# Kernel optimization log

Measured on AMD Instinct MI355X. Metric: run time of the kernel, lower is better.

Reference implementation:

```python
import jax, jax.numpy as jnp
import numpy as np
from jax import lax

EPS = 1e-5  # torch BatchNorm1d default eps

def _conv(x, w, stride):
    # x: [B,H,W,Cin], w: [3,3,Cin,Cout], padding=1
    return lax.conv_general_dilated(x, w, (stride, stride), ((1, 1), (1, 1)),
                                    dimension_numbers=('NHWC', 'HWIO', 'NHWC'))

def _masked_bn(f, m, gamma, beta):
    # BatchNorm1d over active voxels only (training-mode, biased var),
    # matching BN applied to spconv's [N_active, C] feature matrix.
    # f: [B,H,W,C], m: [B,H,W,1] in {0,1}
    cnt = jnp.sum(m)
    mean = jnp.sum(f * m, axis=(0, 1, 2)) / cnt            # [C]
    var = jnp.sum(m * (f - mean) ** 2, axis=(0, 1, 2)) / cnt
    return ((f - mean) * lax.rsqrt(var + EPS) * gamma + beta) * m

def setup_inputs() -> dict:
    key = jax.random.key(0)
    ks = jax.random.split(key, 4)
    B, H, W, Cin, Cout = 4, 256, 256, 64, 128
    x = jax.random.normal(ks[0], (B, H, W, Cin), dtype=jnp.float32)
    mask = jax.random.randint(ks[1], (B, H, W), 0, 10, dtype=jnp.int32)
    w1 = jax.random.normal(ks[2], (3, 3, Cin, Cout), dtype=jnp.float32) * 0.05
    w2 = jax.random.normal(ks[3], (3, 3, Cout, Cout), dtype=jnp.float32) * 0.05
    gamma1 = jnp.ones((Cout,), jnp.float32)
    beta1 = jnp.zeros((Cout,), jnp.float32)
    gamma2 = jnp.ones((Cout,), jnp.float32)
    beta2 = jnp.zeros((Cout,), jnp.float32)
    return {"x": x, "mask": mask, "w1": w1, "gamma1": gamma1, "beta1": beta1,
            "w2": w2, "gamma2": gamma2, "beta2": beta2}

def reference(x, mask, w1, gamma1, beta1, w2, gamma2, beta2):
    act = (mask == 0).astype(x.dtype)[..., None]   # [B,H,W,1] input active sites
    xm = x * act                                   # sparse tensor densified (zeros off-sites)
    # conv1: regular sparse conv, stride 2 -> output active where any input in 3x3 recep. field
    out = _conv(xm, w1, 2)
    m1 = (_conv(act, jnp.ones((3, 3, 1, 1), x.dtype), 2) > 0).astype(x.dtype)
    out = _masked_bn(out, m1, gamma1, beta1)
    out = jax.nn.relu(out)
    # conv2: submanifold conv, stride 1 -> active set preserved (m1)
    out = _conv(out, w2, 1) * m1
    out = _masked_bn(out, m1, gamma2, beta2)
    return out
```

## Files before the change

### kernel.cpp

```cpp
#include <hip/hip_runtime.h>

#define EPS_BN 1e-5f
#define MFMA16 __builtin_amdgcn_mfma_f32_16x16x32_bf16

typedef unsigned char uchar;
typedef short short8 __attribute__((ext_vector_type(8)));
typedef float f32x4 __attribute__((ext_vector_type(4)));

__device__ __forceinline__ ushort f2bf(float f) {
    unsigned u = __float_as_uint(f);
    return (ushort)((u + 0x7FFFu + ((u >> 16) & 1u)) >> 16);
}
__device__ __forceinline__ float bf2f(ushort h) {
    return __uint_as_float(((unsigned)h) << 16);
}
__device__ __forceinline__ void gload_lds16(const void* g, void* l) {
    __builtin_amdgcn_global_load_lds(
        (const __attribute__((address_space(1))) void*)g,
        (__attribute__((address_space(3))) void*)l, 16, 0, 0);
}


__global__ __launch_bounds__(256) void mask_kernel(const int* __restrict__ mask,
                                                   uchar* __restrict__ m1,
                                                   int* __restrict__ cnt)
{
    int idx = blockIdx.x * 256 + threadIdx.x;
    int ow = idx & 127;
    int oh = (idx >> 7) & 127;
    int b  = idx >> 14;
    bool act = false;
    #pragma unroll
    for (int kh = 0; kh < 3; ++kh) {
        int ih = 2*oh - 1 + kh;
        if ((unsigned)ih >= 256u) continue;
        #pragma unroll
        for (int kw = 0; kw < 3; ++kw) {
            int iw = 2*ow - 1 + kw;
            if ((unsigned)iw >= 256u) continue;
            if (mask[(b*256 + ih)*256 + iw] == 0) act = true;
        }
    }
    m1[idx] = act ? 1 : 0;
    unsigned long long bal = __ballot(act);
    if ((threadIdx.x & 63) == 0)
        atomicAdd(cnt, (int)__popcll(bal));
}

__global__ __launch_bounds__(256) void wcvt_kernel(const float* __restrict__ w1,
                                                   const float* __restrict__ w2,
                                                   ushort* __restrict__ w1T,
                                                   ushort* __restrict__ w2T)
{
    int idx = blockIdx.x * 256 + threadIdx.x;
    if (idx < 73728) {
        int ci = idx & 63;
        int co = (idx >> 6) & 127;
        int s  = idx >> 13;
        w1T[idx] = f2bf(w1[(s*64 + ci)*128 + co]);
    } else if (idx < 221184) {
        int i  = idx - 73728;
        int ci = i & 127;
        int co = (i >> 7) & 127;
        int s  = i >> 14;
        w2T[i] = f2bf(w2[(s*128 + ci)*128 + co]);
    }
}

__global__ __launch_bounds__(512) void conv1_mfma(const float* __restrict__ x,
                                                  const int* __restrict__ mask,
                                                  const ushort* __restrict__ w1T,
                                                  const uchar* __restrict__ m1,
                                                  ushort* __restrict__ out1,
                                                  float* __restrict__ stats)
{
    __shared__ ushort Ah[2 * 258 * 64];
    __shared__ ushort Bd[2][8192];

    const int t     = threadIdx.x;
    const int lane  = t & 63;
    const int wv    = t >> 6;
    const int wbase = t & ~63;
    const int bid   = blockIdx.x;
    const int L     = (bid & 7) * 32 + (bid >> 3);
    const int g     = L & 63;
    const int b     = L >> 6;

    const int wm = wv >> 1, wn = wv & 1;
    const int lr = lane & 15, lg = lane >> 4;

    auto stageA = [&](int kh) {
        for (int idx = t; idx < 4128; idx += 512) {
            int r   = idx >= 2064;
            int rem = idx - r*2064;
            int c = rem >> 3, k = rem & 7;
            int iw = c - 1;
            int ih = 4*g + 2*r + kh - 1;
            short8 v = {0,0,0,0,0,0,0,0};
            if ((unsigned)ih < 256u && (unsigned)iw < 256u) {
                const int* mr = mask + (size_t)(b*256 + ih) * 256;
                if (mr[iw] == 0) {
                    const float* p = x + ((size_t)(b*256 + ih)*256 + iw)*64 + k*8;
                    float4 fa = *(const float4*)p;
                    float4 fb = *(const float4*)(p + 4);
                    v[0]=(short)f2bf(fa.x); v[1]=(short)f2bf(fa.y);
                    v[2]=(short)f2bf(fa.z); v[3]=(short)f2bf(fa.w);
                    v[4]=(short)f2bf(fb.x); v[5]=(short)f2bf(fb.y);
                    v[6]=(short)f2bf(fb.z); v[7]=(short)f2bf(fb.w);
                }
            }
            int ad = ((r*258 + c)*128 + k*16) ^ ((((unsigned)c >> 1) & 7) << 4);
            *(short8*)((char*)Ah + ad) = v;
        }
    };
    const int coB = t >> 3;
    const int kB  = t & 7;
    auto dmaB = [&](int buf, int tap) {
        #pragma unroll
        for (int r = 0; r < 2; ++r) {
            int co = r*64 + coB;
            const ushort* gp = w1T + (size_t)tap*8192 + (size_t)co*64
                             + ((kB ^ (co & 7)) << 3);
            gload_lds16(gp, &Bd[buf][(size_t)(r*512 + wbase)*8]);
        }
    };

    f32x4 acc[4][4];
    #pragma unroll
    for (int mi = 0; mi < 4; ++mi)
        #pragma unroll
        for (int ni = 0; ni < 4; ++ni)
            acc[mi][ni] = (f32x4){0.f, 0.f, 0.f, 0.f};

    stageA(0);
    dmaB(0, 0);
    __syncthreads();

    for (int kt = 0; kt < 9; ++kt) {
        const int kw = kt % 3, cb = kt & 1;
        if (kt < 8) dmaB(cb ^ 1, kt + 1);
        const char* Ab = (const char*)Ah;
        const char* Bb = (const char*)Bd[cb];
        __builtin_amdgcn_s_setprio(1);
        #pragma unroll
        for (int ks = 0; ks < 2; ++ks) {
            short8 af[4], bfr[4];
            #pragma unroll
            for (int mi = 0; mi < 4; ++mi) {
                int px = wm*64 + mi*16 + lr;
                int r  = px >> 7, ow = px & 127;
                int c  = 2*ow + kw;
                af[mi] = *(const short8*)(Ab +
                    (((r*258 + c)*128 + ks*64 + lg*16) ^ ((((unsigned)c >> 1) & 7) << 4)));
            }
            #pragma unroll
            for (int ni = 0; ni < 4; ++ni) {
                int co = wn*64 + ni*16 + lr;
                bfr[ni] = *(const short8*)(Bb +
                    ((co*128 + ks*64 + lg*16) ^ ((co & 7) << 4)));
            }
            #pragma unroll
            for (int mi = 0; mi < 4; ++mi)
                #pragma unroll
                for (int ni = 0; ni < 4; ++ni)
                    acc[mi][ni] = MFMA16(af[mi], bfr[ni], acc[mi][ni], 0, 0, 0);
        }
        __builtin_amdgcn_s_setprio(0);
        __syncthreads();
        if (kw == 2 && kt < 8) {
            stageA(kt/3 + 1);
            __syncthreads();
        }
    }

    const size_t pixbase = (size_t)(b*128 + 2*g) * 128;
    #pragma unroll
    for (int mi = 0; mi < 4; ++mi) {
        #pragma unroll
        for (int ni = 0; ni < 4; ++ni) {
            int p  = wm*64 + mi*16 + lg*4;
            int co = wn*64 + ni*16 + lr;
            #pragma unroll
            for (int r = 0; r < 4; ++r)
                out1[(pixbase + p + r)*128 + co] = f2bf(acc[mi][ni][r]);
        }
    }

    float s4[4] = {0.f,0.f,0.f,0.f}, q4[4] = {0.f,0.f,0.f,0.f};
    #pragma unroll
    for (int mi = 0; mi < 4; ++mi) {
        const uchar* mp = m1 + pixbase + wm*64 + mi*16 + lg*4;
        #pragma unroll
        for (int r = 0; r < 4; ++r) {
            float a = mp[r] ? 1.f : 0.f;
            #pragma unroll
            for (int ni = 0; ni < 4; ++ni) {
                float av = a * acc[mi][ni][r];
                s4[ni] += av;
                q4[ni] += av * acc[mi][ni][r];
            }
        }
    }
    float* red = (float*)Ah;
    const int rrow = wm*4 + lg;
    #pragma unroll
    for (int ni = 0; ni < 4; ++ni) {
        red[rrow*128 + wn*64 + ni*16 + lr]        = s4[ni];
        red[2048 + rrow*128 + wn*64 + ni*16 + lr] = q4[ni];
    }
    __syncthreads();
    if (t < 128) {
        float v = 0.f, q = 0.f;
        #pragma unroll
        for (int rr = 0; rr < 16; ++rr) { v += red[rr*128 + t]; q += red[2048 + rr*128 + t]; }
        atomicAdd(&stats[t], v);
        atomicAdd(&stats[128 + t], q);
    }
}

__global__ __launch_bounds__(512) void conv2_mfma(const ushort* __restrict__ a,
                                                  const ushort* __restrict__ w2T,
                                                  const uchar* __restrict__ m1,
                                                  const float* __restrict__ sb,
                                                  float* __restrict__ outraw,
                                                  float* __restrict__ stats)
{
    __shared__ ushort Ah[2 * 130 * 128];
    __shared__ ushort Bd[2][8192];
    __shared__ float scb[256];

    const int t     = threadIdx.x;
    const int lane  = t & 63;
    const int wv    = t >> 6;
    const int wbase = t & ~63;
    const int bid   = blockIdx.x;
    const int L     = (bid & 7) * 32 + (bid >> 3);
    const int g     = L & 63;
    const int b     = L >> 6;

    const int wm = wv >> 1, wn = wv & 1;
    const int lr = lane & 15, lg = lane >> 4;

    if (t < 256) scb[t] = sb[t];

    auto stageA = [&](int kh) {
        for (int idx = t; idx < 4160; idx += 512) {
            int r   = idx >= 2080;
            int rem = idx - r*2080;
            int c = rem >> 4, k = rem & 15;
            int iw = c - 1;
            int ih = 2*g + r + kh - 1;
            short8 v = {0,0,0,0,0,0,0,0};
            if ((unsigned)ih < 128u && (unsigned)iw < 128u) {
                const uchar* mr = m1 + (size_t)(b*128 + ih) * 128;
                if (mr[iw]) {
                    short8 rv = *(const short8*)(a + ((size_t)(b*128 + ih)*128 + iw)*128 + k*8);
                    #pragma unroll
                    for (int j = 0; j < 8; ++j) {
                        float f = fmaf(bf2f((ushort)rv[j]), scb[k*8 + j], scb[128 + k*8 + j]);
                        v[j] = (short)f2bf(fmaxf(f, 0.f));
                    }
                }
            }
            int ad = ((r*130 + c)*256 + k*16) ^ ((c & 7) << 4);
            *(short8*)((char*)Ah + ad) = v;
        }
    };
    const int coB = t >> 3;
    const int kB  = t & 7;
    auto dmaB = [&](int buf, int kt) {
        const int s = kt / 6, j = kt % 6;
        const int tap = s*3 + (j >> 1);
        const int h = j & 1;
        #pragma unroll
        for (int r = 0; r < 2; ++r) {
            int co = r*64 + coB;
            const ushort* gp = w2T + (size_t)tap*16384 + (size_t)co*128 + h*64
                             + ((kB ^ (co & 7)) << 3);
            gload_lds16(gp, &Bd[buf][(size_t)(r*512 + wbase)*8]);
        }
    };

    f32x4 acc[4][4];
    #pragma unroll
    for (int mi = 0; mi < 4; ++mi)
        #pragma unroll
        for (int ni = 0; ni < 4; ++ni)
            acc[mi][ni] = (f32x4){0.f, 0.f, 0.f, 0.f};

    __syncthreads();
    stageA(0);
    dmaB(0, 0);
    __syncthreads();

    for (int kt = 0; kt < 18; ++kt) {
        const int j = kt % 6;
        const int kw = j >> 1, h = j & 1, cb = kt & 1;
        if (kt < 17) dmaB(cb ^ 1, kt + 1);
        const char* Ab = (const char*)Ah;
        const char* Bb = (const char*)Bd[cb];
        __builtin_amdgcn_s_setprio(1);
        #pragma unroll
        for (int ks = 0; ks < 2; ++ks) {
            short8 af[4], bfr[4];
            #pragma unroll
            for (int mi = 0; mi < 4; ++mi) {
                int px = wm*64 + mi*16 + lr;
                int r  = px >> 7, ow = px & 127;
                int c  = ow + kw;
                af[mi] = *(const short8*)(Ab +
                    (((r*130 + c)*256 + h*128 + ks*64 + lg*16) ^ ((c & 7) << 4)));
            }
            #pragma unroll
            for (int ni = 0; ni < 4; ++ni) {
                int co = wn*64 + ni*16 + lr;
                bfr[ni] = *(const short8*)(Bb +
                    ((co*128 + ks*64 + lg*16) ^ ((co & 7) << 4)));
            }
            #pragma unroll
            for (int mi = 0; mi < 4; ++mi)
                #pragma unroll
                for (int ni = 0; ni < 4; ++ni)
                    acc[mi][ni] = MFMA16(af[mi], bfr[ni], acc[mi][ni], 0, 0, 0);
        }
        __builtin_amdgcn_s_setprio(0);
        __syncthreads();
        if (j == 5 && kt < 17) {
            stageA(kt/6 + 1);
            __syncthreads();
        }
    }

    const size_t pixbase = (size_t)(b*128 + 2*g) * 128;
    #pragma unroll
    for (int mi = 0; mi < 4; ++mi) {
        #pragma unroll
        for (int ni = 0; ni < 4; ++ni) {
            int p  = wm*64 + mi*16 + lg*4;
            int co = wn*64 + ni*16 + lr;
            #pragma unroll
            for (int r = 0; r < 4; ++r)
                outraw[(pixbase + p + r)*128 + co] = acc[mi][ni][r];
        }
    }

    float s4[4] = {0.f,0.f,0.f,0.f}, q4[4] = {0.f,0.f,0.f,0.f};
    #pragma unroll
    for (int mi = 0; mi < 4; ++mi) {
        const uchar* mp = m1 + pixbase + wm*64 + mi*16 + lg*4;
        #pragma unroll
        for (int r = 0; r < 4; ++r) {
            float a0 = mp[r] ? 1.f : 0.f;
            #pragma unroll
            for (int ni = 0; ni < 4; ++ni) {
                float av = a0 * acc[mi][ni][r];
                s4[ni] += av;
                q4[ni] += av * acc[mi][ni][r];
            }
        }
    }
    float* red = (float*)Ah;
    const int rrow = wm*4 + lg;
    #pragma unroll
    for (int ni = 0; ni < 4; ++ni) {
        red[rrow*128 + wn*64 + ni*16 + lr]        = s4[ni];
        red[2048 + rrow*128 + wn*64 + ni*16 + lr] = q4[ni];
    }
    __syncthreads();
    if (t < 128) {
        float v = 0.f, q = 0.f;
        #pragma unroll
        for (int rr = 0; rr < 16; ++rr) { v += red[rr*128 + t]; q += red[2048 + rr*128 + t]; }
        atomicAdd(&stats[t], v);
        atomicAdd(&stats[128 + t], q);
    }
}

__global__ void finalize_kernel(const float* __restrict__ stats,
                                const float* __restrict__ gamma,
                                const float* __restrict__ beta,
                                float* __restrict__ sbout,
                                const int* __restrict__ cnt)
{
    int c = threadIdx.x;
    float n = (float)(*cnt);
    float mean = stats[c] / n;
    float var  = stats[128 + c] / n - mean*mean;
    var = fmaxf(var, 0.f);
    float scale = gamma[c] * rsqrtf(var + EPS_BN);
    sbout[c]       = scale;
    sbout[128 + c] = beta[c] - mean*scale;
}

__global__ __launch_bounds__(256) void apply_kernel(float* __restrict__ out,
                                                    const uchar* __restrict__ m1,
                                                    const float* __restrict__ sb)
{
    int idx4 = blockIdx.x * 256 + threadIdx.x;
    int pos = idx4 >> 5;
    int c4  = (idx4 & 31) << 2;
    float4 v = ((const float4*)out)[idx4];
    float4 r = make_float4(0.f, 0.f, 0.f, 0.f);
    if (m1[pos]) {
        r.x = fmaf(v.x, sb[c4+0], sb[128+c4+0]);
        r.y = fmaf(v.y, sb[c4+1], sb[128+c4+1]);
        r.z = fmaf(v.z, sb[c4+2], sb[128+c4+2]);
        r.w = fmaf(v.w, sb[c4+3], sb[128+c4+3]);
    }
    ((float4*)out)[idx4] = r;
}

extern "C" void kernel_launch(void* const* d_in, const int* in_sizes, int n_in,
                              void* d_out, int out_size, void* d_ws, size_t ws_size,
                              hipStream_t stream)
{
    const float* x      = (const float*)d_in[0];
    const int*   mask   = (const int*)d_in[1];
    const float* w1     = (const float*)d_in[2];
    const float* gamma1 = (const float*)d_in[3];
    const float* beta1  = (const float*)d_in[4];
    const float* w2     = (const float*)d_in[5];
    const float* gamma2 = (const float*)d_in[6];
    const float* beta2  = (const float*)d_in[7];

    ushort* out1 = (ushort*)d_ws;
    ushort* w1T  = out1 + 8388608;
    ushort* w2T  = w1T + 73728;
    float* stats = (float*)(w2T + 147456);
    float* sb    = stats + 512;
    int*   cnt   = (int*)(sb + 512);
    uchar* m1    = (uchar*)(cnt + 4);

    float* out = (float*)d_out;

    hipMemsetAsync(stats, 0, 1024*sizeof(float) + 4*sizeof(int), stream);

    mask_kernel <<<256, 256, 0, stream>>>(mask, m1, cnt);
    wcvt_kernel <<<864, 256, 0, stream>>>(w1, w2, w1T, w2T);
    conv1_mfma  <<<256, 512, 0, stream>>>(x, mask, w1T, m1, out1, stats);
    finalize_kernel<<<1, 128, 0, stream>>>(stats, gamma1, beta1, sb, cnt);
    conv2_mfma  <<<256, 512, 0, stream>>>(out1, w2T, m1, sb, out, stats + 256);
    finalize_kernel<<<1, 128, 0, stream>>>(stats + 256, gamma2, beta2, sb + 256, cnt);
    apply_kernel<<<8192, 256, 0, stream>>>(out, m1, sb + 256);
}
```

Baseline: 112.0 us.

## Split conv blocks to one output row each with 256 threads and 512 blocks

Both conv kernels now handle a single output row per block (128 pixels) with 4 waves instead of two rows with 8 waves. The grid doubles to 512 blocks, LDS for the A tile is halved, and the weight DMA is spread over 4 issues per thread. The main loops are fully unrolled and bf16 conversion now uses the HIP library intrinsic. This aims to fill more CUs (256 CUs on MI355X) and raise occupancy, at the cost of loading each weight tile twice as often per output pixel.

```diff
diff --git a/kernel.cpp b/kernel.cpp
--- a/kernel.cpp
+++ b/kernel.cpp
@@ -1,4 +1,5 @@
 #include <hip/hip_runtime.h>
+#include <hip/hip_bf16.h>
 
 #define EPS_BN 1e-5f
 #define MFMA16 __builtin_amdgcn_mfma_f32_16x16x32_bf16
@@ -8,8 +9,8 @@
 typedef float f32x4 __attribute__((ext_vector_type(4)));
 
 __device__ __forceinline__ ushort f2bf(float f) {
-    unsigned u = __float_as_uint(f);
-    return (ushort)((u + 0x7FFFu + ((u >> 16) & 1u)) >> 16);
+    __hip_bfloat16 h = __float2bfloat16(f);
+    return *(ushort*)&h;
 }
 __device__ __forceinline__ float bf2f(ushort h) {
     return __uint_as_float(((unsigned)h) << 16);
@@ -67,14 +68,14 @@
     }
 }
 
-__global__ __launch_bounds__(512) void conv1_mfma(const float* __restrict__ x,
+__global__ __launch_bounds__(256) void conv1_mfma(const float* __restrict__ x,
                                                   const int* __restrict__ mask,
                                                   const ushort* __restrict__ w1T,
                                                   const uchar* __restrict__ m1,
                                                   ushort* __restrict__ out1,
                                                   float* __restrict__ stats)
 {
-    __shared__ ushort Ah[2 * 258 * 64];
+    __shared__ ushort Ah[258 * 64];
     __shared__ ushort Bd[2][8192];
 
     const int t     = threadIdx.x;
@@ -82,34 +83,33 @@
     const int wv    = t >> 6;
     const int wbase = t & ~63;
     const int bid   = blockIdx.x;
-    const int L     = (bid & 7) * 32 + (bid >> 3);
-    const int g     = L & 63;
-    const int b     = L >> 6;
+    const int L     = (bid & 7) * 64 + (bid >> 3);
+    const int oh    = L & 127;
+    const int b     = L >> 7;
 
     const int wm = wv >> 1, wn = wv & 1;
     const int lr = lane & 15, lg = lane >> 4;
 
     auto stageA = [&](int kh) {
-        for (int idx = t; idx < 4128; idx += 512) {
-            int r   = idx >= 2064;
-            int rem = idx - r*2064;
-            int c = rem >> 3, k = rem & 7;
+        int ih = 2*oh + kh - 1;
+        bool rok = ((unsigned)ih < 256u);
+        int ihc = ih < 0 ? 0 : (ih > 255 ? 255 : ih);
+        const float* xr = x + (size_t)(b*256 + ihc) * 256 * 64;
+        const int*   mr = mask + (size_t)(b*256 + ihc) * 256;
+        for (int idx = t; idx < 2064; idx += 256) {
+            int c = idx >> 3, k = idx & 7;
             int iw = c - 1;
-            int ih = 4*g + 2*r + kh - 1;
             short8 v = {0,0,0,0,0,0,0,0};
-            if ((unsigned)ih < 256u && (unsigned)iw < 256u) {
-                const int* mr = mask + (size_t)(b*256 + ih) * 256;
-                if (mr[iw] == 0) {
-                    const float* p = x + ((size_t)(b*256 + ih)*256 + iw)*64 + k*8;
-                    float4 fa = *(const float4*)p;
-                    float4 fb = *(const float4*)(p + 4);
-                    v[0]=(short)f2bf(fa.x); v[1]=(short)f2bf(fa.y);
-                    v[2]=(short)f2bf(fa.z); v[3]=(short)f2bf(fa.w);
-                    v[4]=(short)f2bf(fb.x); v[5]=(short)f2bf(fb.y);
-                    v[6]=(short)f2bf(fb.z); v[7]=(short)f2bf(fb.w);
-                }
-            }
-            int ad = ((r*258 + c)*128 + k*16) ^ ((((unsigned)c >> 1) & 7) << 4);
+            if (rok && (unsigned)iw < 256u && mr[iw] == 0) {
+                const float* p = xr + (size_t)iw*64 + k*8;
+                float4 fa = *(const float4*)p;
+                float4 fb = *(const float4*)(p + 4);
+                v[0]=(short)f2bf(fa.x); v[1]=(short)f2bf(fa.y);
+                v[2]=(short)f2bf(fa.z); v[3]=(short)f2bf(fa.w);
+                v[4]=(short)f2bf(fb.x); v[5]=(short)f2bf(fb.y);
+                v[6]=(short)f2bf(fb.z); v[7]=(short)f2bf(fb.w);
+            }
+            int ad = (c*128 + k*16) ^ ((((unsigned)c >> 1) & 7) << 4);
             *(short8*)((char*)Ah + ad) = v;
         }
     };
@@ -117,11 +117,11 @@
     const int kB  = t & 7;
     auto dmaB = [&](int buf, int tap) {
         #pragma unroll
-        for (int r = 0; r < 2; ++r) {
-            int co = r*64 + coB;
+        for (int r = 0; r < 4; ++r) {
+            int co = r*32 + coB;
             const ushort* gp = w1T + (size_t)tap*8192 + (size_t)co*64
                              + ((kB ^ (co & 7)) << 3);
-            gload_lds16(gp, &Bd[buf][(size_t)(r*512 + wbase)*8]);
+            gload_lds16(gp, &Bd[buf][(size_t)(r*256 + wbase)*8]);
         }
     };
 
@@ -136,6 +136,7 @@
     dmaB(0, 0);
     __syncthreads();
 
+    #pragma unroll
     for (int kt = 0; kt < 9; ++kt) {
         const int kw = kt % 3, cb = kt & 1;
         if (kt < 8) dmaB(cb ^ 1, kt + 1);
@@ -148,10 +149,9 @@
             #pragma unroll
             for (int mi = 0; mi < 4; ++mi) {
                 int px = wm*64 + mi*16 + lr;
-                int r  = px >> 7, ow = px & 127;
-                int c  = 2*ow + kw;
+                int c  = 2*px + kw;
                 af[mi] = *(const short8*)(Ab +
-                    (((r*258 + c)*128 + ks*64 + lg*16) ^ ((((unsigned)c >> 1) & 7) << 4)));
+                    ((c*128 + ks*64 + lg*16) ^ ((((unsigned)c >> 1) & 7) << 4)));
             }
             #pragma unroll
             for (int ni = 0; ni < 4; ++ni) {
@@ -173,7 +173,7 @@
         }
     }
 
-    const size_t pixbase = (size_t)(b*128 + 2*g) * 128;
+    const size_t pixbase = (size_t)(b*128 + oh) * 128;
     #pragma unroll
     for (int mi = 0; mi < 4; ++mi) {
         #pragma unroll
@@ -206,26 +206,26 @@
     #pragma unroll
     for (int ni = 0; ni < 4; ++ni) {
         red[rrow*128 + wn*64 + ni*16 + lr]        = s4[ni];
-        red[2048 + rrow*128 + wn*64 + ni*16 + lr] = q4[ni];
+        red[1024 + rrow*128 + wn*64 + ni*16 + lr] = q4[ni];
     }
     __syncthreads();
     if (t < 128) {
         float v = 0.f, q = 0.f;
         #pragma unroll
-        for (int rr = 0; rr < 16; ++rr) { v += red[rr*128 + t]; q += red[2048 + rr*128 + t]; }
+        for (int rr = 0; rr < 8; ++rr) { v += red[rr*128 + t]; q += red[1024 + rr*128 + t]; }
         atomicAdd(&stats[t], v);
         atomicAdd(&stats[128 + t], q);
     }
 }
 
-__global__ __launch_bounds__(512) void conv2_mfma(const ushort* __restrict__ a,
+__global__ __launch_bounds__(256) void conv2_mfma(const ushort* __restrict__ a,
                                                   const ushort* __restrict__ w2T,
                                                   const uchar* __restrict__ m1,
                                                   const float* __restrict__ sb,
                                                   float* __restrict__ outraw,
                                                   float* __restrict__ stats)
 {
-    __shared__ ushort Ah[2 * 130 * 128];
+    __shared__ ushort Ah[130 * 128];
     __shared__ ushort Bd[2][8192];
     __shared__ float scb[256];
 
@@ -234,35 +234,34 @@
     const int wv    = t >> 6;
     const int wbase = t & ~63;
     const int bid   = blockIdx.x;
-    const int L     = (bid & 7) * 32 + (bid >> 3);
-    const int g     = L & 63;
-    const int b     = L >> 6;
+    const int L     = (bid & 7) * 64 + (bid >> 3);
+    const int oh    = L & 127;
+    const int b     = L >> 7;
 
     const int wm = wv >> 1, wn = wv & 1;
     const int lr = lane & 15, lg = lane >> 4;
 
-    if (t < 256) scb[t] = sb[t];
+    scb[t & 255] = sb[t & 255];
 
     auto stageA = [&](int kh) {
-        for (int idx = t; idx < 4160; idx += 512) {
-            int r   = idx >= 2080;
-            int rem = idx - r*2080;
-            int c = rem >> 4, k = rem & 15;
+        int ih = oh + kh - 1;
+        bool rok = ((unsigned)ih < 128u);
+        int ihc = ih < 0 ? 0 : (ih > 127 ? 127 : ih);
+        const ushort* ar = a + (size_t)(b*128 + ihc) * 128 * 128;
+        const uchar*  mr = m1 + (size_t)(b*128 + ihc) * 128;
+        for (int idx = t; idx < 2080; idx += 256) {
+            int c = idx >> 4, k = idx & 15;
             int iw = c - 1;
-            int ih = 2*g + r + kh - 1;
             short8 v = {0,0,0,0,0,0,0,0};
-            if ((unsigned)ih < 128u && (unsigned)iw < 128u) {
-                const uchar* mr = m1 + (size_t)(b*128 + ih) * 128;
-                if (mr[iw]) {
-                    short8 rv = *(const short8*)(a + ((size_t)(b*128 + ih)*128 + iw)*128 + k*8);
-                    #pragma unroll
-                    for (int j = 0; j < 8; ++j) {
-                        float f = fmaf(bf2f((ushort)rv[j]), scb[k*8 + j], scb[128 + k*8 + j]);
-                        v[j] = (short)f2bf(fmaxf(f, 0.f));
-                    }
+            if (rok && (unsigned)iw < 128u && mr[iw]) {
+                short8 rv = *(const short8*)(ar + (size_t)iw*128 + k*8);
+                #pragma unroll
+                for (int j = 0; j < 8; ++j) {
+                    float f = fmaf(bf2f((ushort)rv[j]), scb[k*8 + j], scb[128 + k*8 + j]);
+                    v[j] = (short)f2bf(fmaxf(f, 0.f));
                 }
             }
-            int ad = ((r*130 + c)*256 + k*16) ^ ((c & 7) << 4);
+            int ad = (c*256 + k*16) ^ ((c & 7) << 4);
             *(short8*)((char*)Ah + ad) = v;
         }
     };
@@ -273,11 +272,11 @@
         const int tap = s*3 + (j >> 1);
         const int h = j & 1;
         #pragma unroll
-        for (int r = 0; r < 2; ++r) {
-            int co = r*64 + coB;
+        for (int r = 0; r < 4; ++r) {
+            int co = r*32 + coB;
             const ushort* gp = w2T + (size_t)tap*16384 + (size_t)co*128 + h*64
                              + ((kB ^ (co & 7)) << 3);
-            gload_lds16(gp, &Bd[buf][(size_t)(r*512 + wbase)*8]);
+            gload_lds16(gp, &Bd[buf][(size_t)(r*256 + wbase)*8]);
         }
     };
 
@@ -293,6 +292,7 @@
     dmaB(0, 0);
     __syncthreads();
 
+    #pragma unroll
     for (int kt = 0; kt < 18; ++kt) {
         const int j = kt % 6;
         const int kw = j >> 1, h = j & 1, cb = kt & 1;
@@ -306,10 +306,9 @@
             #pragma unroll
             for (int mi = 0; mi < 4; ++mi) {
                 int px = wm*64 + mi*16 + lr;
-                int r  = px >> 7, ow = px & 127;
-                int c  = ow + kw;
+                int c  = px + kw;
                 af[mi] = *(const short8*)(Ab +
-                    (((r*130 + c)*256 + h*128 + ks*64 + lg*16) ^ ((c & 7) << 4)));
+                    ((c*256 + h*128 + ks*64 + lg*16) ^ ((c & 7) << 4)));
             }
             #pragma unroll
             for (int ni = 0; ni < 4; ++ni) {
@@ -331,7 +330,7 @@
         }
     }
 
-    const size_t pixbase = (size_t)(b*128 + 2*g) * 128;
+    const size_t pixbase = (size_t)(b*128 + oh) * 128;
     #pragma unroll
     for (int mi = 0; mi < 4; ++mi) {
         #pragma unroll
@@ -364,13 +363,13 @@
     #pragma unroll
     for (int ni = 0; ni < 4; ++ni) {
         red[rrow*128 + wn*64 + ni*16 + lr]        = s4[ni];
-        red[2048 + rrow*128 + wn*64 + ni*16 + lr] = q4[ni];
+        red[1024 + rrow*128 + wn*64 + ni*16 + lr] = q4[ni];
     }
     __syncthreads();
     if (t < 128) {
         float v = 0.f, q = 0.f;
         #pragma unroll
-        for (int rr = 0; rr < 16; ++rr) { v += red[rr*128 + t]; q += red[2048 + rr*128 + t]; }
+        for (int rr = 0; rr < 8; ++rr) { v += red[rr*128 + t]; q += red[1024 + rr*128 + t]; }
         atomicAdd(&stats[t], v);
         atomicAdd(&stats[128 + t], q);
     }
@@ -437,9 +436,9 @@
 
     mask_kernel <<<256, 256, 0, stream>>>(mask, m1, cnt);
     wcvt_kernel <<<864, 256, 0, stream>>>(w1, w2, w1T, w2T);
-    conv1_mfma  <<<256, 512, 0, stream>>>(x, mask, w1T, m1, out1, stats);
+    conv1_mfma  <<<512, 256, 0, stream>>>(x, mask, w1T, m1, out1, stats);
     finalize_kernel<<<1, 128, 0, stream>>>(stats, gamma1, beta1, sb, cnt);
-    conv2_mfma  <<<256, 512, 0, stream>>>(out1, w2T, m1, sb, out, stats + 256);
+    conv2_mfma  <<<512, 256, 0, stream>>>(out1, w2T, m1, sb, out, stats + 256);
     finalize_kernel<<<1, 128, 0, stream>>>(stats + 256, gamma2, beta2, sb + 256, cnt);
     apply_kernel<<<8192, 256, 0, stream>>>(out, m1, sb + 256);
 }
```

New measurement: 111.6 us. Within noise of the previous version (-0.4%).

## Triple-buffer weight DMA with explicit vmcnt waits in both conv kernels

Applied to the files above, without the earlier changes.

Replaces double-buffered weight tile loads with a three-deep ring buffer, prefetching two taps ahead. Full __syncthreads are replaced by targeted s_waitcnt vmcnt/lgkmcnt plus raw barriers so more global loads stay in flight during MFMA work. The K loops are fully unrolled, and bf16 rounding now uses the HIP intrinsic. This adds LDS usage, which may lower occupancy, and the correctness of the hand-written wait counts depends on how stageA issues its loads.

```diff
diff --git a/kernel.cpp b/kernel.cpp
--- a/kernel.cpp
+++ b/kernel.cpp
@@ -1,15 +1,20 @@
 #include <hip/hip_runtime.h>
+#include <hip/hip_bf16.h>
 
 #define EPS_BN 1e-5f
 #define MFMA16 __builtin_amdgcn_mfma_f32_16x16x32_bf16
+#define VW2 do { asm volatile("s_waitcnt vmcnt(2)" ::: "memory"); __builtin_amdgcn_sched_barrier(0); } while(0)
+#define VW4 do { asm volatile("s_waitcnt vmcnt(4)" ::: "memory"); __builtin_amdgcn_sched_barrier(0); } while(0)
+#define LK0 do { asm volatile("s_waitcnt lgkmcnt(0)" ::: "memory"); __builtin_amdgcn_sched_barrier(0); } while(0)
+#define SBAR __builtin_amdgcn_s_barrier()
 
 typedef unsigned char uchar;
 typedef short short8 __attribute__((ext_vector_type(8)));
 typedef float f32x4 __attribute__((ext_vector_type(4)));
 
 __device__ __forceinline__ ushort f2bf(float f) {
-    unsigned u = __float_as_uint(f);
-    return (ushort)((u + 0x7FFFu + ((u >> 16) & 1u)) >> 16);
+    __hip_bfloat16 h = __float2bfloat16(f);
+    return *(ushort*)&h;
 }
 __device__ __forceinline__ float bf2f(ushort h) {
     return __uint_as_float(((unsigned)h) << 16);
@@ -75,7 +80,7 @@
                                                   float* __restrict__ stats)
 {
     __shared__ ushort Ah[2 * 258 * 64];
-    __shared__ ushort Bd[2][8192];
+    __shared__ ushort Bd[3][8192];
 
     const int t     = threadIdx.x;
     const int lane  = t & 63;
@@ -133,12 +138,14 @@
             acc[mi][ni] = (f32x4){0.f, 0.f, 0.f, 0.f};
 
     stageA(0);
-    dmaB(0, 0);
-    __syncthreads();
-
+    dmaB(0, 0); dmaB(1, 1); dmaB(2, 2);
+    VW4;
+    LK0;
+    SBAR;
+
+    #pragma unroll
     for (int kt = 0; kt < 9; ++kt) {
-        const int kw = kt % 3, cb = kt & 1;
-        if (kt < 8) dmaB(cb ^ 1, kt + 1);
+        const int kw = kt % 3, cb = kt % 3;
         const char* Ab = (const char*)Ah;
         const char* Bb = (const char*)Bd[cb];
         __builtin_amdgcn_s_setprio(1);
@@ -166,12 +173,18 @@
                     acc[mi][ni] = MFMA16(af[mi], bfr[ni], acc[mi][ni], 0, 0, 0);
         }
         __builtin_amdgcn_s_setprio(0);
-        __syncthreads();
-        if (kw == 2 && kt < 8) {
-            stageA(kt/3 + 1);
-            __syncthreads();
-        }
-    }
+        if (kt < 8) {
+            VW2;
+            SBAR;
+            if (kt <= 5) dmaB(kt % 3, kt + 3);
+            if (kw == 2) {
+                stageA(kt/3 + 1);
+                LK0;
+                SBAR;
+            }
+        }
+    }
+    __syncthreads();
 
     const size_t pixbase = (size_t)(b*128 + 2*g) * 128;
     #pragma unroll
@@ -226,7 +239,7 @@
                                                   float* __restrict__ stats)
 {
     __shared__ ushort Ah[2 * 130 * 128];
-    __shared__ ushort Bd[2][8192];
+    __shared__ ushort Bd[3][8192];
     __shared__ float scb[256];
 
     const int t     = threadIdx.x;
@@ -290,13 +303,15 @@
 
     __syncthreads();
     stageA(0);
-    dmaB(0, 0);
-    __syncthreads();
-
+    dmaB(0, 0); dmaB(1, 1); dmaB(2, 2);
+    VW4;
+    LK0;
+    SBAR;
+
+    #pragma unroll
     for (int kt = 0; kt < 18; ++kt) {
         const int j = kt % 6;
-        const int kw = j >> 1, h = j & 1, cb = kt & 1;
-        if (kt < 17) dmaB(cb ^ 1, kt + 1);
+        const int kw = j >> 1, h = j & 1, cb = kt % 3;
         const char* Ab = (const char*)Ah;
         const char* Bb = (const char*)Bd[cb];
         __builtin_amdgcn_s_setprio(1);
@@ -324,12 +339,18 @@
                     acc[mi][ni] = MFMA16(af[mi], bfr[ni], acc[mi][ni], 0, 0, 0);
         }
         __builtin_amdgcn_s_setprio(0);
-        __syncthreads();
-        if (j == 5 && kt < 17) {
-            stageA(kt/6 + 1);
-            __syncthreads();
-        }
-    }
+        if (kt < 17) {
+            VW2;
+            SBAR;
+            if (kt <= 14) dmaB(kt % 3, kt + 3);
+            if (j == 5) {
+                stageA(kt/6 + 1);
+                LK0;
+                SBAR;
+            }
+        }
+    }
+    __syncthreads();
 
     const size_t pixbase = (size_t)(b*128 + 2*g) * 128;
     #pragma unroll
```

Measured after the change: 105.7 us. -5.7%, faster.

## Interleave weight DMA with MFMA subtiles using explicit waitcnt and barriers

Applied to the files above, without the earlier changes.

Splits each B-tile prefetch into two halves issued per k-substep, and replaces __syncthreads with explicit s_waitcnt plus raw s_barrier so each wave waits only on the counters it needs. Two barriers per substep let every wave's fragment reads land before the MFMA burst, meant to overlap global-to-LDS weight loads with matrix work more finely. It also swaps the manual float-to-bf16 rounding for the HIP intrinsic. The extra barriers per substep add synchronisation cost, and hand-placed waitcnts risk hazards if the compiler reorders memory operations.

```diff
diff --git a/kernel.cpp b/kernel.cpp
--- a/kernel.cpp
+++ b/kernel.cpp
@@ -1,15 +1,19 @@
 #include <hip/hip_runtime.h>
+#include <hip/hip_bf16.h>
 
 #define EPS_BN 1e-5f
 #define MFMA16 __builtin_amdgcn_mfma_f32_16x16x32_bf16
+#define VW0 do { asm volatile("s_waitcnt vmcnt(0)" ::: "memory"); __builtin_amdgcn_sched_barrier(0); } while(0)
+#define LK0 do { asm volatile("s_waitcnt lgkmcnt(0)" ::: "memory"); __builtin_amdgcn_sched_barrier(0); } while(0)
+#define SBAR __builtin_amdgcn_s_barrier()
 
 typedef unsigned char uchar;
 typedef short short8 __attribute__((ext_vector_type(8)));
 typedef float f32x4 __attribute__((ext_vector_type(4)));
 
 __device__ __forceinline__ ushort f2bf(float f) {
-    unsigned u = __float_as_uint(f);
-    return (ushort)((u + 0x7FFFu + ((u >> 16) & 1u)) >> 16);
+    __hip_bfloat16 h = __float2bfloat16(f);
+    return *(ushort*)&h;
 }
 __device__ __forceinline__ float bf2f(ushort h) {
     return __uint_as_float(((unsigned)h) << 16);
@@ -115,14 +119,11 @@
     };
     const int coB = t >> 3;
     const int kB  = t & 7;
-    auto dmaB = [&](int buf, int tap) {
-        #pragma unroll
-        for (int r = 0; r < 2; ++r) {
-            int co = r*64 + coB;
-            const ushort* gp = w1T + (size_t)tap*8192 + (size_t)co*64
-                             + ((kB ^ (co & 7)) << 3);
-            gload_lds16(gp, &Bd[buf][(size_t)(r*512 + wbase)*8]);
-        }
+    auto dmaB1 = [&](int buf, int tap, int r) {
+        int co = r*64 + coB;
+        const ushort* gp = w1T + (size_t)tap*8192 + (size_t)co*64
+                         + ((kB ^ (co & 7)) << 3);
+        gload_lds16(gp, &Bd[buf][(size_t)(r*512 + wbase)*8]);
     };
 
     f32x4 acc[4][4];
@@ -133,15 +134,15 @@
             acc[mi][ni] = (f32x4){0.f, 0.f, 0.f, 0.f};
 
     stageA(0);
-    dmaB(0, 0);
-    __syncthreads();
+    dmaB1(0, 0, 0); dmaB1(0, 0, 1);
+    LK0;
+    VW0;
+    SBAR;
 
     for (int kt = 0; kt < 9; ++kt) {
         const int kw = kt % 3, cb = kt & 1;
-        if (kt < 8) dmaB(cb ^ 1, kt + 1);
         const char* Ab = (const char*)Ah;
         const char* Bb = (const char*)Bd[cb];
-        __builtin_amdgcn_s_setprio(1);
         #pragma unroll
         for (int ks = 0; ks < 2; ++ks) {
             short8 af[4], bfr[4];
@@ -159,19 +160,26 @@
                 bfr[ni] = *(const short8*)(Bb +
                     ((co*128 + ks*64 + lg*16) ^ ((co & 7) << 4)));
             }
+            if (kt < 8) dmaB1(cb ^ 1, kt + 1, ks);
+            SBAR;
+            LK0;
+            __builtin_amdgcn_s_setprio(1);
             #pragma unroll
             for (int mi = 0; mi < 4; ++mi)
                 #pragma unroll
                 for (int ni = 0; ni < 4; ++ni)
                     acc[mi][ni] = MFMA16(af[mi], bfr[ni], acc[mi][ni], 0, 0, 0);
-        }
-        __builtin_amdgcn_s_setprio(0);
-        __syncthreads();
+            __builtin_amdgcn_s_setprio(0);
+            if (ks == 1 && kt < 8) VW0;
+            SBAR;
+        }
         if (kw == 2 && kt < 8) {
             stageA(kt/3 + 1);
-            __syncthreads();
-        }
-    }
+            LK0;
+            SBAR;
+        }
+    }
+    __syncthreads();
 
     const size_t pixbase = (size_t)(b*128 + 2*g) * 128;
     #pragma unroll
@@ -268,17 +276,14 @@
     };
     const int coB = t >> 3;
     const int kB  = t & 7;
-    auto dmaB = [&](int buf, int kt) {
+    auto dmaB1 = [&](int buf, int kt, int r) {
         const int s = kt / 6, j = kt % 6;
         const int tap = s*3 + (j >> 1);
         const int h = j & 1;
-        #pragma unroll
-        for (int r = 0; r < 2; ++r) {
-            int co = r*64 + coB;
-            const ushort* gp = w2T + (size_t)tap*16384 + (size_t)co*128 + h*64
-                             + ((kB ^ (co & 7)) << 3);
-            gload_lds16(gp, &Bd[buf][(size_t)(r*512 + wbase)*8]);
-        }
+        int co = r*64 + coB;
+        const ushort* gp = w2T + (size_t)tap*16384 + (size_t)co*128 + h*64
+                         + ((kB ^ (co & 7)) << 3);
+        gload_lds16(gp, &Bd[buf][(size_t)(r*512 + wbase)*8]);
     };
 
     f32x4 acc[4][4];
@@ -290,16 +295,16 @@
 
     __syncthreads();
     stageA(0);
-    dmaB(0, 0);
-    __syncthreads();
+    dmaB1(0, 0, 0); dmaB1(0, 0, 1);
+    LK0;
+    VW0;
+    SBAR;
 
     for (int kt = 0; kt < 18; ++kt) {
         const int j = kt % 6;
         const int kw = j >> 1, h = j & 1, cb = kt & 1;
-        if (kt < 17) dmaB(cb ^ 1, kt + 1);
         const char* Ab = (const char*)Ah;
         const char* Bb = (const char*)Bd[cb];
-        __builtin_amdgcn_s_setprio(1);
         #pragma unroll
         for (int ks = 0; ks < 2; ++ks) {
             short8 af[4], bfr[4];
@@ -317,19 +322,26 @@
                 bfr[ni] = *(const short8*)(Bb +
                     ((co*128 + ks*64 + lg*16) ^ ((co & 7) << 4)));
             }
+            if (kt < 17) dmaB1(cb ^ 1, kt + 1, ks);
+            SBAR;
+            LK0;
+            __builtin_amdgcn_s_setprio(1);
             #pragma unroll
             for (int mi = 0; mi < 4; ++mi)
                 #pragma unroll
                 for (int ni = 0; ni < 4; ++ni)
                     acc[mi][ni] = MFMA16(af[mi], bfr[ni], acc[mi][ni], 0, 0, 0);
-        }
-        __builtin_amdgcn_s_setprio(0);
-        __syncthreads();
+            __builtin_amdgcn_s_setprio(0);
+            if (ks == 1 && kt < 17) VW0;
+            SBAR;
+        }
         if (j == 5 && kt < 17) {
             stageA(kt/6 + 1);
-            __syncthreads();
-        }
-    }
+            LK0;
+            SBAR;
+        }
+    }
+    __syncthreads();
 
     const size_t pixbase = (size_t)(b*128 + 2*g) * 128;
     #pragma unroll
```

After: 113.8 us. No clear change (+1.6%).
